# Kernel optimization log

Hardware: AMD Instinct MI355X
Metric: run time of the kernel (lower is better)

Reference implementation:

```python
import jax, jax.numpy as jnp
import numpy as np

N_NODES = 40000
N_EDGES = 640000
D = 128
D_OUT = 128


def _layernorm(x, gamma, beta, eps=1e-5):
    mu = jnp.mean(x, axis=-1, keepdims=True)
    var = jnp.mean(jnp.square(x - mu), axis=-1, keepdims=True)
    return (x - mu) * jax.lax.rsqrt(var + eps) * gamma + beta


def setup_inputs() -> dict:
    key = jax.random.key(0)
    ks = jax.random.split(key, 6)
    x = jax.random.normal(ks[0], (N_NODES, D), dtype=jnp.float32)
    edge_index = jax.random.randint(ks[1], (2, N_EDGES), 0, N_NODES, dtype=jnp.int64)
    s = 1.0 / np.sqrt(D)
    return {
        "x": x,
        "edge_index": edge_index,
        "ln1_w": jnp.ones((D,), jnp.float32),
        "ln1_b": jnp.zeros((D,), jnp.float32),
        "ln2_w": jnp.ones((D,), jnp.float32),
        "ln2_b": jnp.zeros((D,), jnp.float32),
        "w": jnp.ones((D,), jnp.float32),
        "W1": jax.random.normal(ks[2], (D, D), jnp.float32) * s,
        "W2": jax.random.normal(ks[3], (D, D), jnp.float32) * s,
        "O1": jax.random.normal(ks[4], (2 * D, D), jnp.float32) * s,
        "O2": jax.random.normal(ks[5], (D, D_OUT), jnp.float32) * s,
    }


def reference(x, edge_index, ln1_w, ln1_b, ln2_w, ln2_b, w, W1, W2, O1, O2):
    row, col = edge_index[0], edge_index[1]
    n = x.shape[0]
    # gather + 2-layer message MLP (bias-free): [E, D]
    msg = jnp.maximum(x[row] @ W1, 0.0) @ W2
    # scatter_mean over destination nodes (zero where no incoming edges)
    agg = jax.ops.segment_sum(msg, col, num_segments=n)
    cnt = jax.ops.segment_sum(jnp.ones((msg.shape[0],), x.dtype), col, num_segments=n)
    agg = agg / jnp.maximum(cnt, 1.0)[:, None]
    agg_n = _layernorm(agg, ln1_w, ln1_b)
    # repulsion + residual + LayerNorm
    fx = _layernorm(x + (x - agg_n) * w, ln2_w, ln2_b)
    # concat + output MLP
    cat = jnp.concatenate([fx, agg_n], axis=1)
    return jnp.maximum(cat @ O1, 0.0) @ O2
```

## Files before the change

kernel.cpp:

```cpp
#include <hip/hip_runtime.h>
#include <hip/hip_bf16.h>

#define NN 40000
#define NE 640000
#define DD 128
#define CAP 64
#define FILLB 250

typedef __attribute__((ext_vector_type(8))) short bf16x8;
typedef __attribute__((ext_vector_type(8))) unsigned short u16x8;
typedef __attribute__((ext_vector_type(4))) float f32x4;

__device__ __forceinline__ unsigned short f2bf(float f) {
    __hip_bfloat16 h = __float2bfloat16(f);
    return *reinterpret_cast<unsigned short*>(&h);
}
__device__ __forceinline__ float bf2f(unsigned short u) {
    union { unsigned int ui; float f; } v;
    v.ui = ((unsigned int)u) << 16;
    return v.f;
}
__device__ __forceinline__ void gload16(void* lds, const void* g) {
    __builtin_amdgcn_global_load_lds(
        (const __attribute__((address_space(1))) void*)g,
        (__attribute__((address_space(3))) void*)lds, 16, 0, 0);
}

__global__ __launch_bounds__(256) void prep_kernel(
    const float* __restrict__ W1, const float* __restrict__ W2,
    const float* __restrict__ O1, const float* __restrict__ O2,
    unsigned short* __restrict__ w1t, unsigned short* __restrict__ w2t,
    unsigned short* __restrict__ o1t, unsigned short* __restrict__ o2t,
    unsigned int* __restrict__ cnt)
{
    int bx = blockIdx.x;
    if (bx >= 320) {
        int t = (bx - 320) * 256 + threadIdx.x;
        if (t < NN) cnt[t] = 0u;
        return;
    }
    int t = bx * 256 + threadIdx.x;
    if (t < 16384) {
        int n = t >> 7, k = t & 127;
        unsigned b = (unsigned)(n * 256) + (((unsigned)(k * 2)) ^ (((unsigned)(n & 7)) << 4));
        w1t[b >> 1] = f2bf(W1[k * 128 + n]);
    } else if (t < 32768) {
        int i = t - 16384;
        int n = i >> 7, k = i & 127;
        unsigned b = (unsigned)(n * 256) + (((unsigned)(k * 2)) ^ (((unsigned)(n & 7)) << 4));
        w2t[b >> 1] = f2bf(W2[k * 128 + n]);
    } else if (t < 65536) {
        int i = t - 32768;
        int n = i >> 8, k = i & 255;
        unsigned b = (unsigned)(n * 512 + (k >> 7) * 256)
                   + (((unsigned)((k & 127) * 2)) ^ (((unsigned)(n & 7)) << 4));
        o1t[b >> 1] = f2bf(O1[k * 128 + n]);
    } else {
        int i = t - 65536;
        int n = i >> 7, k = i & 127;
        unsigned b = (unsigned)(n * 256) + (((unsigned)(k * 2)) ^ (((unsigned)(n & 7)) << 4));
        o2t[b >> 1] = f2bf(O2[k * 128 + n]);
    }
}

__global__ __launch_bounds__(256) void mega1_kernel(
    const float* __restrict__ x, const unsigned short* __restrict__ w1t,
    const unsigned short* __restrict__ w2t, unsigned short* __restrict__ nm,
    const int* __restrict__ ei, unsigned int* __restrict__ cnt,
    unsigned short* __restrict__ srcs)
{
    __shared__ unsigned short xt[64 * 128];
    __shared__ unsigned short wb[128 * 128];
    const int tid = threadIdx.x;
    const int bx = blockIdx.x;

    if (bx >= 625) {
        const int base = (bx - 625) * 2560 + tid;
        int s[10], d[10];
        #pragma unroll
        for (int j = 0; j < 10; ++j) d[j] = ei[NE + base + j * 256];
        #pragma unroll
        for (int j = 0; j < 10; ++j) s[j] = ei[base + j * 256];
        unsigned int p[10];
        #pragma unroll
        for (int j = 0; j < 10; ++j) p[j] = atomicAdd(cnt + d[j], 1u);
        #pragma unroll
        for (int j = 0; j < 10; ++j)
            if (p[j] < CAP)
                __builtin_nontemporal_store((unsigned short)s[j],
                                            srcs + (size_t)d[j] * CAP + p[j]);
        return;
    }

    const int row0 = bx * 64;
    const int lane = tid & 63;
    const int wv = tid >> 6;

    #pragma unroll
    for (int it = 0; it < 8; ++it) {
        int b = (wv * 8 + it) * 1024;
        gload16((char*)wb + b, (const char*)w1t + b + lane * 16);
    }
    #pragma unroll
    for (int it = 0; it < 4; ++it) {
        int c = tid + it * 256;
        int r = c >> 4;
        int c0 = (c & 15) << 3;
        const float4* gp = reinterpret_cast<const float4*>(x + (size_t)(row0 + r) * DD + c0);
        float4 f0 = gp[0], f1 = gp[1];
        u16x8 p;
        p[0] = f2bf(f0.x); p[1] = f2bf(f0.y); p[2] = f2bf(f0.z); p[3] = f2bf(f0.w);
        p[4] = f2bf(f1.x); p[5] = f2bf(f1.y); p[6] = f2bf(f1.z); p[7] = f2bf(f1.w);
        unsigned b = (unsigned)((r * DD + c0) * 2) ^ ((unsigned)(r & 7) << 4);
        *reinterpret_cast<u16x8*>(reinterpret_cast<char*>(xt) + b) = p;
    }
    __syncthreads();

    const int l15 = lane & 15;
    const int lg = lane >> 4;

    f32x4 acc[8];
    #pragma unroll
    for (int i = 0; i < 8; ++i) acc[i] = (f32x4){0.f, 0.f, 0.f, 0.f};

    #pragma unroll
    for (int kk = 0; kk < 4; ++kk) {
        int k = kk * 32 + lg * 8;
        int ar = wv * 16 + l15;
        bf16x8 a = *reinterpret_cast<const bf16x8*>(
            reinterpret_cast<const char*>(xt) + ((unsigned)((ar * DD + k) * 2) ^ ((unsigned)(ar & 7) << 4)));
        #pragma unroll
        for (int n0 = 0; n0 < 8; ++n0) {
            int bn = n0 * 16 + l15;
            bf16x8 bf = *reinterpret_cast<const bf16x8*>(
                reinterpret_cast<const char*>(wb) + ((unsigned)((bn * DD + k) * 2) ^ ((unsigned)(bn & 7) << 4)));
            acc[n0] = __builtin_amdgcn_mfma_f32_16x16x32_bf16(a, bf, acc[n0], 0, 0, 0);
        }
    }
    __syncthreads();

    #pragma unroll
    for (int it = 0; it < 8; ++it) {
        int b = (wv * 8 + it) * 1024;
        gload16((char*)wb + b, (const char*)w2t + b + lane * 16);
    }
    unsigned short* hb = xt;
    #pragma unroll
    for (int n0 = 0; n0 < 8; ++n0) {
        #pragma unroll
        for (int ri = 0; ri < 4; ++ri) {
            int r = wv * 16 + lg * 4 + ri;
            int cc = n0 * 16 + l15;
            float v = fmaxf(acc[n0][ri], 0.0f);
            *reinterpret_cast<unsigned short*>(
                reinterpret_cast<char*>(hb) + ((unsigned)((r * DD + cc) * 2) ^ ((unsigned)(r & 7) << 4))) = f2bf(v);
        }
    }
    __syncthreads();

    f32x4 acc2[8];
    #pragma unroll
    for (int i = 0; i < 8; ++i) acc2[i] = (f32x4){0.f, 0.f, 0.f, 0.f};
    #pragma unroll
    for (int kk = 0; kk < 4; ++kk) {
        int k = kk * 32 + lg * 8;
        int ar = wv * 16 + l15;
        bf16x8 a = *reinterpret_cast<const bf16x8*>(
            reinterpret_cast<const char*>(hb) + ((unsigned)((ar * DD + k) * 2) ^ ((unsigned)(ar & 7) << 4)));
        #pragma unroll
        for (int n0 = 0; n0 < 8; ++n0) {
            int bn = n0 * 16 + l15;
            bf16x8 bf = *reinterpret_cast<const bf16x8*>(
                reinterpret_cast<const char*>(wb) + ((unsigned)((bn * DD + k) * 2) ^ ((unsigned)(bn & 7) << 4)));
            acc2[n0] = __builtin_amdgcn_mfma_f32_16x16x32_bf16(a, bf, acc2[n0], 0, 0, 0);
        }
    }
    #pragma unroll
    for (int n0 = 0; n0 < 8; ++n0) {
        #pragma unroll
        for (int ri = 0; ri < 4; ++ri) {
            int r = row0 + wv * 16 + lg * 4 + ri;
            int cc = n0 * 16 + l15;
            nm[(size_t)r * DD + cc] = f2bf(acc2[n0][ri]);
        }
    }
}

__global__ __launch_bounds__(256) void pull_node_kernel(
    const unsigned short* __restrict__ nm, const unsigned short* __restrict__ srcs,
    const unsigned int* __restrict__ cnt,
    const float* __restrict__ x,
    const float* __restrict__ g1, const float* __restrict__ b1,
    const float* __restrict__ g2, const float* __restrict__ b2,
    const float* __restrict__ w, unsigned short* __restrict__ catb)
{
    const int lane = threadIdx.x & 63;
    const int wv = threadIdx.x >> 6;
    const int i = blockIdx.x * 4 + wv;
    const int d0 = lane * 2;

    const unsigned int degf = cnt[i];
    const int deg = (int)(degf < CAP ? degf : CAP);
    const unsigned short* sp = srcs + (size_t)i * CAP;

    float a0 = 0.f, a1 = 0.f;
    int e = 0;
    for (; e + 8 <= deg; e += 8) {
        int s[8];
        #pragma unroll
        for (int j = 0; j < 8; ++j) s[j] = sp[e + j];
        ushort2 m[8];
        #pragma unroll
        for (int j = 0; j < 8; ++j)
            m[j] = *reinterpret_cast<const ushort2*>(nm + (size_t)s[j] * DD + d0);
        #pragma unroll
        for (int j = 0; j < 8; ++j) { a0 += bf2f(m[j].x); a1 += bf2f(m[j].y); }
    }
    for (; e + 4 <= deg; e += 4) {
        int s0 = sp[e + 0], s1 = sp[e + 1], s2 = sp[e + 2], s3 = sp[e + 3];
        ushort2 m0 = *reinterpret_cast<const ushort2*>(nm + (size_t)s0 * DD + d0);
        ushort2 m1 = *reinterpret_cast<const ushort2*>(nm + (size_t)s1 * DD + d0);
        ushort2 m2 = *reinterpret_cast<const ushort2*>(nm + (size_t)s2 * DD + d0);
        ushort2 m3 = *reinterpret_cast<const ushort2*>(nm + (size_t)s3 * DD + d0);
        a0 += bf2f(m0.x) + bf2f(m1.x) + bf2f(m2.x) + bf2f(m3.x);
        a1 += bf2f(m0.y) + bf2f(m1.y) + bf2f(m2.y) + bf2f(m3.y);
    }
    for (; e < deg; ++e) {
        int s0 = sp[e];
        ushort2 m0 = *reinterpret_cast<const ushort2*>(nm + (size_t)s0 * DD + d0);
        a0 += bf2f(m0.x);
        a1 += bf2f(m0.y);
    }

    float inv = 1.0f / fmaxf((float)degf, 1.0f);
    a0 *= inv; a1 *= inv;

    float s = a0 + a1;
    #pragma unroll
    for (int o = 32; o > 0; o >>= 1) s += __shfl_xor(s, o, 64);
    float mu = s * (1.0f / 128.0f);
    float e0 = a0 - mu, e1 = a1 - mu;
    float q = e0 * e0 + e1 * e1;
    #pragma unroll
    for (int o = 32; o > 0; o >>= 1) q += __shfl_xor(q, o, 64);
    float rs = rsqrtf(q * (1.0f / 128.0f) + 1e-5f);

    float2 g1v = *reinterpret_cast<const float2*>(g1 + d0);
    float2 b1v = *reinterpret_cast<const float2*>(b1 + d0);
    float an0 = e0 * rs * g1v.x + b1v.x;
    float an1 = e1 * rs * g1v.y + b1v.y;

    float2 xv = *reinterpret_cast<const float2*>(x + (size_t)i * DD + d0);
    float2 wv2 = *reinterpret_cast<const float2*>(w + d0);
    float t0 = xv.x + (xv.x - an0) * wv2.x;
    float t1 = xv.y + (xv.y - an1) * wv2.y;

    float s2 = t0 + t1;
    #pragma unroll
    for (int o = 32; o > 0; o >>= 1) s2 += __shfl_xor(s2, o, 64);
    float mu2 = s2 * (1.0f / 128.0f);
    float f0 = t0 - mu2, f1 = t1 - mu2;
    float q2 = f0 * f0 + f1 * f1;
    #pragma unroll
    for (int o = 32; o > 0; o >>= 1) q2 += __shfl_xor(q2, o, 64);
    float rs2 = rsqrtf(q2 * (1.0f / 128.0f) + 1e-5f);

    float2 g2v = *reinterpret_cast<const float2*>(g2 + d0);
    float2 b2v = *reinterpret_cast<const float2*>(b2 + d0);
    float fx0 = f0 * rs2 * g2v.x + b2v.x;
    float fx1 = f1 * rs2 * g2v.y + b2v.y;

    ushort2 uo; uo.x = f2bf(fx0); uo.y = f2bf(fx1);
    *reinterpret_cast<ushort2*>(catb + (size_t)i * 256 + d0) = uo;
    ushort2 ua; ua.x = f2bf(an0); ua.y = f2bf(an1);
    *reinterpret_cast<ushort2*>(catb + (size_t)i * 256 + 128 + d0) = ua;
}

__global__ __launch_bounds__(256) void mlp2_kernel(
    const unsigned short* __restrict__ catb, const unsigned short* __restrict__ o1t,
    const unsigned short* __restrict__ o2t, float* __restrict__ out)
{
    __shared__ unsigned short ct[64 * 128];
    __shared__ unsigned short wb[128 * 128];
    const int tid = threadIdx.x;
    const int row0 = blockIdx.x * 64;
    const int lane = tid & 63;
    const int wv = tid >> 6;
    const int l15 = lane & 15;
    const int lg = lane >> 4;

    f32x4 acc[8];
    #pragma unroll
    for (int i = 0; i < 8; ++i) acc[i] = (f32x4){0.f, 0.f, 0.f, 0.f};

    for (int h = 0; h < 2; ++h) {
        #pragma unroll
        for (int it = 0; it < 8; ++it) {
            int Lb = (wv * 8 + it) * 1024;
            int n = (Lb >> 8) + (lane >> 4);
            int c2 = (lane & 15) * 16;
            gload16((char*)wb + Lb, (const char*)o1t + n * 512 + h * 256 + c2);
        }
        #pragma unroll
        for (int it = 0; it < 4; ++it) {
            int c = tid + it * 256;
            int r = c >> 4;
            int c0 = (c & 15) << 3;
            u16x8 v = *reinterpret_cast<const u16x8*>(catb + (size_t)(row0 + r) * 256 + h * 128 + c0);
            unsigned b = (unsigned)((r * 128 + c0) * 2) ^ ((unsigned)(r & 7) << 4);
            *reinterpret_cast<u16x8*>(reinterpret_cast<char*>(ct) + b) = v;
        }
        __syncthreads();
        #pragma unroll
        for (int kk = 0; kk < 4; ++kk) {
            int k = kk * 32 + lg * 8;
            int ar = wv * 16 + l15;
            bf16x8 a = *reinterpret_cast<const bf16x8*>(
                reinterpret_cast<const char*>(ct) + ((unsigned)((ar * 128 + k) * 2) ^ ((unsigned)(ar & 7) << 4)));
            #pragma unroll
            for (int n0 = 0; n0 < 8; ++n0) {
                int bn = n0 * 16 + l15;
                bf16x8 bf = *reinterpret_cast<const bf16x8*>(
                    reinterpret_cast<const char*>(wb) + ((unsigned)((bn * 128 + k) * 2) ^ ((unsigned)(bn & 7) << 4)));
                acc[n0] = __builtin_amdgcn_mfma_f32_16x16x32_bf16(a, bf, acc[n0], 0, 0, 0);
            }
        }
        __syncthreads();
    }

    #pragma unroll
    for (int it = 0; it < 8; ++it) {
        int b = (wv * 8 + it) * 1024;
        gload16((char*)wb + b, (const char*)o2t + b + lane * 16);
    }
    unsigned short* hb = ct;
    #pragma unroll
    for (int n0 = 0; n0 < 8; ++n0) {
        #pragma unroll
        for (int ri = 0; ri < 4; ++ri) {
            int r = wv * 16 + lg * 4 + ri;
            int cc = n0 * 16 + l15;
            float v = fmaxf(acc[n0][ri], 0.0f);
            *reinterpret_cast<unsigned short*>(
                reinterpret_cast<char*>(hb) + ((unsigned)((r * DD + cc) * 2) ^ ((unsigned)(r & 7) << 4))) = f2bf(v);
        }
    }
    __syncthreads();

    f32x4 acc2[8];
    #pragma unroll
    for (int i = 0; i < 8; ++i) acc2[i] = (f32x4){0.f, 0.f, 0.f, 0.f};
    #pragma unroll
    for (int kk = 0; kk < 4; ++kk) {
        int k = kk * 32 + lg * 8;
        int ar = wv * 16 + l15;
        bf16x8 a = *reinterpret_cast<const bf16x8*>(
            reinterpret_cast<const char*>(hb) + ((unsigned)((ar * DD + k) * 2) ^ ((unsigned)(ar & 7) << 4)));
        #pragma unroll
        for (int n0 = 0; n0 < 8; ++n0) {
            int bn = n0 * 16 + l15;
            bf16x8 bf = *reinterpret_cast<const bf16x8*>(
                reinterpret_cast<const char*>(wb) + ((unsigned)((bn * DD + k) * 2) ^ ((unsigned)(bn & 7) << 4)));
            acc2[n0] = __builtin_amdgcn_mfma_f32_16x16x32_bf16(a, bf, acc2[n0], 0, 0, 0);
        }
    }

    #pragma unroll
    for (int n0 = 0; n0 < 8; ++n0) {
        #pragma unroll
        for (int ri = 0; ri < 4; ++ri) {
            int r = row0 + wv * 16 + lg * 4 + ri;
            int cc = n0 * 16 + l15;
            out[(size_t)r * DD + cc] = acc2[n0][ri];
        }
    }
}

extern "C" void kernel_launch(void* const* d_in, const int* in_sizes, int n_in,
                              void* d_out, int out_size, void* d_ws, size_t ws_size,
                              hipStream_t stream) {
    const float* x   = (const float*)d_in[0];
    const int*   ei  = (const int*)d_in[1];
    const float* g1  = (const float*)d_in[2];
    const float* b1  = (const float*)d_in[3];
    const float* g2  = (const float*)d_in[4];
    const float* b2  = (const float*)d_in[5];
    const float* w   = (const float*)d_in[6];
    const float* W1  = (const float*)d_in[7];
    const float* W2  = (const float*)d_in[8];
    const float* O1  = (const float*)d_in[9];
    const float* O2  = (const float*)d_in[10];
    float* out = (float*)d_out;

    char* ws = (char*)d_ws;
    unsigned short* nm   = (unsigned short*)(ws);
    unsigned short* catb = (unsigned short*)(ws + 10240000);
    unsigned short* srcs = (unsigned short*)(ws + 30720000);
    unsigned int*   cnt  = (unsigned int*)(ws + 35840000);
    unsigned short* w1t  = (unsigned short*)(ws + 36000000);
    unsigned short* w2t  = (unsigned short*)(ws + 36032768);
    unsigned short* o1t  = (unsigned short*)(ws + 36065536);
    unsigned short* o2t  = (unsigned short*)(ws + 36131072);

    prep_kernel<<<477, 256, 0, stream>>>(W1, W2, O1, O2, w1t, w2t, o1t, o2t, cnt);
    mega1_kernel<<<625 + FILLB, 256, 0, stream>>>(x, w1t, w2t, nm, ei, cnt, srcs);
    pull_node_kernel<<<NN / 4, 256, 0, stream>>>(nm, srcs, cnt, x, g1, b1, g2, b2, w, catb);
    mlp2_kernel<<<NN / 64, 256, 0, stream>>>(catb, o1t, o2t, out);
}
```

Before: 178.3 us.

## Split edge fill out of fused MLP kernel and pad degree counters per cache line

Moves the edge bucketing (atomic degree count plus source scatter) out of the fused mega kernel into its own fill kernel, launched before a now pure MLP1 kernel. The per-node counters are spread out with a 16-word stride so each counter sits on its own 64-byte line, which is meant to reduce atomic contention and false sharing. The source scatter now uses regular stores instead of nontemporal ones. The cost is losing the overlap of atomic-heavy fill work with the MFMA blocks, plus one extra launch and a larger counter footprint.

After: 170.1 us. -4.6%, faster.

```diff
diff --git a/kernel.cpp b/kernel.cpp
--- a/kernel.cpp
+++ b/kernel.cpp
@@ -5,7 +5,6 @@
 #define NE 640000
 #define DD 128
 #define CAP 64
-#define FILLB 250
 
 typedef __attribute__((ext_vector_type(8))) short bf16x8;
 typedef __attribute__((ext_vector_type(8))) unsigned short u16x8;
@@ -36,7 +35,7 @@
     int bx = blockIdx.x;
     if (bx >= 320) {
         int t = (bx - 320) * 256 + threadIdx.x;
-        if (t < NN) cnt[t] = 0u;
+        if (t < NN) cnt[t * 16] = 0u;
         return;
     }
     int t = bx * 256 + threadIdx.x;
@@ -63,36 +62,14 @@
     }
 }
 
-__global__ __launch_bounds__(256) void mega1_kernel(
+__global__ __launch_bounds__(256) void mlp1_kernel(
     const float* __restrict__ x, const unsigned short* __restrict__ w1t,
-    const unsigned short* __restrict__ w2t, unsigned short* __restrict__ nm,
-    const int* __restrict__ ei, unsigned int* __restrict__ cnt,
-    unsigned short* __restrict__ srcs)
+    const unsigned short* __restrict__ w2t, unsigned short* __restrict__ nm)
 {
     __shared__ unsigned short xt[64 * 128];
     __shared__ unsigned short wb[128 * 128];
     const int tid = threadIdx.x;
-    const int bx = blockIdx.x;
-
-    if (bx >= 625) {
-        const int base = (bx - 625) * 2560 + tid;
-        int s[10], d[10];
-        #pragma unroll
-        for (int j = 0; j < 10; ++j) d[j] = ei[NE + base + j * 256];
-        #pragma unroll
-        for (int j = 0; j < 10; ++j) s[j] = ei[base + j * 256];
-        unsigned int p[10];
-        #pragma unroll
-        for (int j = 0; j < 10; ++j) p[j] = atomicAdd(cnt + d[j], 1u);
-        #pragma unroll
-        for (int j = 0; j < 10; ++j)
-            if (p[j] < CAP)
-                __builtin_nontemporal_store((unsigned short)s[j],
-                                            srcs + (size_t)d[j] * CAP + p[j]);
-        return;
-    }
-
-    const int row0 = bx * 64;
+    const int row0 = blockIdx.x * 64;
     const int lane = tid & 63;
     const int wv = tid >> 6;
 
@@ -184,6 +161,24 @@
             nm[(size_t)r * DD + cc] = f2bf(acc2[n0][ri]);
         }
     }
+}
+
+__global__ __launch_bounds__(256) void fill_kernel(
+    const int* __restrict__ ei, unsigned int* __restrict__ cnt,
+    unsigned short* __restrict__ srcs)
+{
+    const int t = blockIdx.x * 256 + threadIdx.x;
+    int s[4], d[4];
+    #pragma unroll
+    for (int j = 0; j < 4; ++j) d[j] = ei[NE + t + j * 160000];
+    #pragma unroll
+    for (int j = 0; j < 4; ++j) s[j] = ei[t + j * 160000];
+    unsigned int p[4];
+    #pragma unroll
+    for (int j = 0; j < 4; ++j) p[j] = atomicAdd(cnt + d[j] * 16, 1u);
+    #pragma unroll
+    for (int j = 0; j < 4; ++j)
+        if (p[j] < CAP) srcs[(size_t)d[j] * CAP + p[j]] = (unsigned short)s[j];
 }
 
 __global__ __launch_bounds__(256) void pull_node_kernel(
@@ -199,7 +194,7 @@
     const int i = blockIdx.x * 4 + wv;
     const int d0 = lane * 2;
 
-    const unsigned int degf = cnt[i];
+    const unsigned int degf = cnt[i * 16];
     const int deg = (int)(degf < CAP ? degf : CAP);
     const unsigned short* sp = srcs + (size_t)i * CAP;
 
@@ -397,13 +392,14 @@
     unsigned short* catb = (unsigned short*)(ws + 10240000);
     unsigned short* srcs = (unsigned short*)(ws + 30720000);
     unsigned int*   cnt  = (unsigned int*)(ws + 35840000);
-    unsigned short* w1t  = (unsigned short*)(ws + 36000000);
-    unsigned short* w2t  = (unsigned short*)(ws + 36032768);
-    unsigned short* o1t  = (unsigned short*)(ws + 36065536);
-    unsigned short* o2t  = (unsigned short*)(ws + 36131072);
+    unsigned short* w1t  = (unsigned short*)(ws + 38400000);
+    unsigned short* w2t  = (unsigned short*)(ws + 38432768);
+    unsigned short* o1t  = (unsigned short*)(ws + 38465536);
+    unsigned short* o2t  = (unsigned short*)(ws + 38531072);
 
     prep_kernel<<<477, 256, 0, stream>>>(W1, W2, O1, O2, w1t, w2t, o1t, o2t, cnt);
-    mega1_kernel<<<625 + FILLB, 256, 0, stream>>>(x, w1t, w2t, nm, ei, cnt, srcs);
+    fill_kernel<<<625, 256, 0, stream>>>(ei, cnt, srcs);
+    mlp1_kernel<<<625, 256, 0, stream>>>(x, w1t, w2t, nm);
     pull_node_kernel<<<NN / 4, 256, 0, stream>>>(nm, srcs, cnt, x, g1, b1, g2, b2, w, catb);
     mlp2_kernel<<<NN / 64, 256, 0, stream>>>(catb, o1t, o2t, out);
 }
```
